# Kernel optimization log

Measured on AMD Instinct MI355X. Metric: run time of the kernel, lower is better.

Reference implementation:

```python
import jax, jax.numpy as jnp
import numpy as np

FP8_MAX = 448.0  # float8_e4m3 max finite value


def setup_inputs() -> dict:
    key = jax.random.key(0)
    k1, k2, k3, k4, k5 = jax.random.split(key, 5)
    B, S, IN, OUT = 8, 2048, 2048, 2048
    x = jax.random.normal(k1, (B, S, IN), dtype=jnp.float32)
    weight = jax.random.normal(k2, (OUT, IN), dtype=jnp.float32) * 0.02
    bias = jax.random.normal(k3, (OUT,), dtype=jnp.float32)
    # per-tensor scales, kept positive and away from zero
    scale_in = jax.random.uniform(k4, (1,), dtype=jnp.float32) * 0.09 + 0.01
    scale_w = jax.random.uniform(k5, (1,), dtype=jnp.float32) * 0.09 + 0.01
    return {"x": x, "weight": weight, "bias": bias,
            "scale_in": scale_in, "scale_w": scale_w}


def _fp8_quantize(x, scale):
    # divide by scale, saturate to fp8 range, cast to fp8 e4m3
    q = jnp.clip(x / scale, -FP8_MAX, FP8_MAX)
    return q.astype(jnp.float8_e4m3fn)


def reference(x, weight, bias, scale_in, scale_w):
    # quantize input and weight to fp8 (per-tensor scales)
    xq = _fp8_quantize(x, scale_in)            # [B,S,IN] fp8
    wq = _fp8_quantize(weight, scale_w)        # [OUT,IN] fp8
    # scaled matmul: accumulate in fp32, dequant with scale_a*scale_b, emit fp16
    acc = jnp.einsum('bsk,nk->bsn', xq.astype(jnp.float32), wq.astype(jnp.float32))
    out = (acc * (scale_in[0] * scale_w[0])).astype(jnp.float16)
    out = out + bias.astype(jnp.float16)       # trailing bias add at fp16
    return out
```

## Files before the change

### kernel.cpp

```cpp
#include <hip/hip_runtime.h>
#include <hip/hip_fp16.h>
#include <stdint.h>

#define MDIM 16384
#define NDIM 2048
#define KDIM 2048

typedef __attribute__((ext_vector_type(4))) float f32x4;
typedef __attribute__((ext_vector_type(4))) int   i32x4;
typedef __attribute__((ext_vector_type(8))) int   i32x8;

__device__ __forceinline__ unsigned f32_to_e4m3(float x) {
    float q = fminf(448.f, fmaxf(-448.f, x));
    unsigned ub = __float_as_uint(q);
    unsigned sgn = (ub >> 24) & 0x80u;
    float aq = fabsf(q);
    int E = (int)((__float_as_uint(aq) >> 23) & 0xff) - 127;
    if (E < -6) E = -6;
    float rq = __uint_as_float((unsigned)(130 - E) << 23);
    int m = (int)rintf(aq * rq);
    if (m == 16) { m = 8; E += 1; }
    unsigned bits;
    if (m < 8) bits = sgn | (unsigned)m;
    else       bits = sgn | ((unsigned)(E + 7) << 3) | (unsigned)(m - 8);
    return bits;
}

__device__ __forceinline__ void quant_span(const float* __restrict__ x,
                                           uint8_t* __restrict__ q, float sc,
                                           unsigned i0, unsigned stride,
                                           unsigned n16) {
    for (unsigned i = i0; i < n16; i += stride) {
        const float4* xp = (const float4*)(x + (size_t)i * 16);
        uint32_t w[4];
#pragma unroll
        for (int j = 0; j < 4; ++j) {
            float4 v = xp[j];
            unsigned b0 = f32_to_e4m3(v.x / sc);
            unsigned b1 = f32_to_e4m3(v.y / sc);
            unsigned b2 = f32_to_e4m3(v.z / sc);
            unsigned b3 = f32_to_e4m3(v.w / sc);
            w[j] = b0 | (b1 << 8) | (b2 << 16) | (b3 << 24);
        }
        ((uint4*)q)[i] = make_uint4(w[0], w[1], w[2], w[3]);
    }
}

__global__ void quant_both_kernel(const float* __restrict__ x,
                                  uint8_t* __restrict__ xq,
                                  const float* __restrict__ w,
                                  uint8_t* __restrict__ wq,
                                  const float* __restrict__ s_in,
                                  const float* __restrict__ s_w) {
    if (blockIdx.x < 2048) {
        unsigned i0 = blockIdx.x * blockDim.x + threadIdx.x;
        quant_span(x, xq, s_in[0], i0, 2048 * 256,
                   (unsigned)((size_t)MDIM * KDIM / 16));
    } else {
        unsigned i0 = (blockIdx.x - 2048) * blockDim.x + threadIdx.x;
        quant_span(w, wq, s_w[0], i0, 256 * 256,
                   (unsigned)((size_t)NDIM * KDIM / 16));
    }
}

#define BM 256
#define BN 256
#define BKB 128
#define NKT (KDIM / BKB)

__device__ __forceinline__ void gload_lds16(const uint8_t* g, uint8_t* l) {
    __builtin_amdgcn_global_load_lds(
        (const __attribute__((address_space(1))) void*)g,
        (__attribute__((address_space(3))) void*)l, 16, 0, 0);
}

__device__ __forceinline__ void barrier_fenced() {
    asm volatile("" ::: "memory");
    __builtin_amdgcn_s_barrier();
    asm volatile("" ::: "memory");
}

__global__ __launch_bounds__(512) void gemm_fp8_kernel(
    const uint8_t* __restrict__ Aq, const uint8_t* __restrict__ Bq,
    const float* __restrict__ bias, const float* __restrict__ s_in,
    const float* __restrict__ s_w, float* __restrict__ out) {

    extern __shared__ uint8_t lds[];

    int nwg = gridDim.x;
    int cpx = nwg >> 3;
    int bid = blockIdx.x;
    int swz = (bid & 7) * cpx + (bid >> 3);
    int tm = swz >> 3;
    int tn = swz & 7;
    int row0 = tm * BM;
    int col0 = tn * BN;

    int tid  = threadIdx.x;
    int lane = tid & 63;
    int wid  = tid >> 6;
    int wr = wid >> 2, wc = wid & 3;
    int r15 = lane & 15;
    int g   = lane >> 4;

    int perm0 = ((2 * g + r15) & 7) << 4;
    int perm1 = ((2 * g + 1 + r15) & 7) << 4;

    int pj[2] = {tid, 512 + tid};
    int rj[2], cj[2];
#pragma unroll
    for (int j = 0; j < 2; ++j) {
        rj[j] = pj[j] >> 3;
        cj[j] = ((pj[j] & 7) - (rj[j] & 7)) & 7;
    }
    size_t asrcoff[2], bsrcoff[2];
    int    adst[2], bdst[2];
#pragma unroll
    for (int j = 0; j < 2; ++j) {
        int ar = (rj[j] & 63) + ((rj[j] >> 6) << 7);
        asrcoff[j] = (size_t)ar * KDIM + cj[j] * 16;
        bsrcoff[j] = (size_t)rj[j] * KDIM + cj[j] * 16;
        adst[j] = pj[j] * 16;
        bdst[j] = 32768 + pj[j] * 16;
    }

    const uint8_t* Asrc = Aq + (size_t)row0 * KDIM;
    const uint8_t* Bsrc = Bq + (size_t)col0 * KDIM;

#define STAGE_A(U, KT, DST)                                                   \
    {                                                                         \
        _Pragma("unroll")                                                     \
        for (int j_ = 0; j_ < 2; ++j_)                                        \
            gload_lds16(Asrc + asrcoff[j_] + (size_t)(U) * 64 * KDIM +        \
                            (size_t)(KT) * BKB,                               \
                        (DST) + adst[j_] + (U) * 16384);                      \
    }
#define STAGE_B(U, KT, DST)                                                   \
    {                                                                         \
        _Pragma("unroll")                                                     \
        for (int j_ = 0; j_ < 2; ++j_)                                        \
            gload_lds16(Bsrc + bsrcoff[j_] + (size_t)(U) * 128 * KDIM +       \
                            (size_t)(KT) * BKB,                               \
                        (DST) + bdst[j_] + (U) * 16384);                      \
    }

    f32x4 acc[8][4];
#pragma unroll
    for (int m = 0; m < 8; ++m)
#pragma unroll
        for (int n = 0; n < 4; ++n)
            acc[m][n] = (f32x4){0.f, 0.f, 0.f, 0.f};

    {
        uint8_t* b0 = &lds[0];
        uint8_t* b1 = &lds[65536];
        STAGE_A(0, 0, b0); STAGE_B(0, 0, b0); STAGE_B(1, 0, b0); STAGE_A(1, 0, b0);
        STAGE_A(0, 1, b1); STAGE_B(0, 1, b1);
        asm volatile("s_waitcnt vmcnt(4)" ::: "memory");
        barrier_fenced();
    }

    int aRowBase = wr * 64;
    int bUnit = (wc >> 1) * 1024;
    int bRowBase = (wc & 1) * 64;

    i32x8 bf[4], af[4];

#define LOAD_BF(bo)                                                           \
    _Pragma("unroll")                                                         \
    for (int n_ = 0; n_ < 4; ++n_) {                                          \
        int rB = bRowBase + n_ * 16 + r15;                                    \
        const uint8_t* rp = lds + (bo) + 32768 + (bUnit + rB * 8) * 16;       \
        i32x4 lo = *(const i32x4*)(rp + perm0);                               \
        i32x4 hi = *(const i32x4*)(rp + perm1);                               \
        _Pragma("unroll")                                                     \
        for (int q_ = 0; q_ < 4; ++q_) { bf[n_][q_] = lo[q_]; bf[n_][4 + q_] = hi[q_]; } \
    }

#define LOAD_AF(bo, MH)                                                       \
    _Pragma("unroll")                                                         \
    for (int m_ = 0; m_ < 4; ++m_) {                                          \
        int rA = aRowBase + m_ * 16 + r15;                                    \
        const uint8_t* rp = lds + (bo) + ((MH) * 1024 + rA * 8) * 16;         \
        i32x4 lo = *(const i32x4*)(rp + perm0);                               \
        i32x4 hi = *(const i32x4*)(rp + perm1);                               \
        _Pragma("unroll")                                                     \
        for (int q_ = 0; q_ < 4; ++q_) { af[m_][q_] = lo[q_]; af[m_][4 + q_] = hi[q_]; } \
    }

#define MFMA_BLOCK(MH)                                                        \
    __builtin_amdgcn_s_setprio(1);                                            \
    _Pragma("unroll")                                                         \
    for (int m_ = 0; m_ < 4; ++m_)                                            \
        _Pragma("unroll")                                                     \
        for (int n_ = 0; n_ < 4; ++n_)                                        \
            acc[(MH) * 4 + m_][n_] =                                          \
                __builtin_amdgcn_mfma_scale_f32_16x16x128_f8f6f4(             \
                    af[m_], bf[n_], acc[(MH) * 4 + m_][n_],                   \
                    0, 0, 0, 127, 0, 127);                                    \
    __builtin_amdgcn_s_setprio(0);

    for (int t = 0; t < NKT; ++t) {
        const unsigned bo = (unsigned)(t & 1) << 16;
        uint8_t* nbuf = &lds[(unsigned)((t + 1) & 1) << 16];
        uint8_t* cbuf = &lds[bo];
        if (t + 1 < NKT) { STAGE_B(1, t + 1, nbuf); STAGE_A(1, t + 1, nbuf); }
        LOAD_BF(bo);
        LOAD_AF(bo, 0);
        MFMA_BLOCK(0);
        barrier_fenced();
        if (t + 2 < NKT) { STAGE_A(0, t + 2, cbuf); STAGE_B(0, t + 2, cbuf); }
        LOAD_AF(bo, 1);
        MFMA_BLOCK(1);
        if (t + 2 < NKT)      asm volatile("s_waitcnt vmcnt(4)" ::: "memory");
        else if (t + 1 < NKT) asm volatile("s_waitcnt vmcnt(0)" ::: "memory");
        barrier_fenced();
    }

    float s = s_in[0] * s_w[0];
    int g4 = g * 4;
#pragma unroll
    for (int n = 0; n < 4; ++n) {
        int col = col0 + wc * 64 + n * 16 + r15;
        __half hb = __float2half(bias[col]);
#pragma unroll
        for (int mh = 0; mh < 2; ++mh)
#pragma unroll
            for (int m = 0; m < 4; ++m) {
                int rbase = row0 + wr * 128 + mh * 64 + m * 16 + g4;
#pragma unroll
                for (int r = 0; r < 4; ++r) {
                    __half h = __float2half(acc[mh * 4 + m][n][r] * s);
                    out[(size_t)(rbase + r) * NDIM + col] =
                        __half2float(__hadd(h, hb));
                }
            }
    }
#undef STAGE_A
#undef STAGE_B
#undef LOAD_BF
#undef LOAD_AF
#undef MFMA_BLOCK
}

extern "C" void kernel_launch(void* const* d_in, const int* in_sizes, int n_in,
                              void* d_out, int out_size, void* d_ws, size_t ws_size,
                              hipStream_t stream) {
    const float* x      = (const float*)d_in[0];
    const float* weight = (const float*)d_in[1];
    const float* bias   = (const float*)d_in[2];
    const float* s_in   = (const float*)d_in[3];
    const float* s_w    = (const float*)d_in[4];
    float* out          = (float*)d_out;

    uint8_t* xq = (uint8_t*)d_ws;
    uint8_t* wq = (uint8_t*)d_ws + (size_t)MDIM * KDIM;

    quant_both_kernel<<<2304, 256, 0, stream>>>(x, xq, weight, wq, s_in, s_w);

    dim3 grid((MDIM / BM) * (NDIM / BN));
    gemm_fp8_kernel<<<grid, 512, 131072, stream>>>(xq, wq, bias, s_in, s_w, out);
}
```

Before: 119.6 us.

## Re-pipeline K loop with one-tile prefetch and stage epilogue through LDS

The main loop is restructured so the next K tile is prefetched into the other LDS buffer in pieces that are interleaved between quarter-sized MFMA groups, instead of a two-tiles-ahead split across buffer halves. B fragments are loaded in halves, and the waitcnt and barrier points are moved to match. The epilogue now writes scaled, bias-added results into an LDS slab and then stores full rows with 16-byte vector writes, replacing the strided per-element global stores. This adds extra barriers and LDS traffic in the epilogue, and the shorter prefetch distance may expose more global-load latency.

```diff
diff --git a/kernel.cpp b/kernel.cpp
--- a/kernel.cpp
+++ b/kernel.cpp
@@ -153,10 +153,8 @@
 
     {
         uint8_t* b0 = &lds[0];
-        uint8_t* b1 = &lds[65536];
-        STAGE_A(0, 0, b0); STAGE_B(0, 0, b0); STAGE_B(1, 0, b0); STAGE_A(1, 0, b0);
-        STAGE_A(0, 1, b1); STAGE_B(0, 1, b1);
-        asm volatile("s_waitcnt vmcnt(4)" ::: "memory");
+        STAGE_A(0, 0, b0); STAGE_B(1, 0, b0); STAGE_B(0, 0, b0); STAGE_A(1, 0, b0);
+        asm volatile("s_waitcnt vmcnt(2)" ::: "memory");
         barrier_fenced();
     }
 
@@ -166,9 +164,9 @@
 
     i32x8 bf[4], af[4];
 
-#define LOAD_BF(bo)                                                           \
+#define LOAD_BF_H(bo, H)                                                      \
     _Pragma("unroll")                                                         \
-    for (int n_ = 0; n_ < 4; ++n_) {                                          \
+    for (int n_ = 2 * (H); n_ < 2 * (H) + 2; ++n_) {                          \
         int rB = bRowBase + n_ * 16 + r15;                                    \
         const uint8_t* rp = lds + (bo) + 32768 + (bUnit + rB * 8) * 16;       \
         i32x4 lo = *(const i32x4*)(rp + perm0);                               \
@@ -188,12 +186,12 @@
         for (int q_ = 0; q_ < 4; ++q_) { af[m_][q_] = lo[q_]; af[m_][4 + q_] = hi[q_]; } \
     }
 
-#define MFMA_BLOCK(MH)                                                        \
+#define MFMA_Q(MH, NH)                                                        \
     __builtin_amdgcn_s_setprio(1);                                            \
     _Pragma("unroll")                                                         \
     for (int m_ = 0; m_ < 4; ++m_)                                            \
         _Pragma("unroll")                                                     \
-        for (int n_ = 0; n_ < 4; ++n_)                                        \
+        for (int n_ = 2 * (NH); n_ < 2 * (NH) + 2; ++n_)                      \
             acc[(MH) * 4 + m_][n_] =                                          \
                 __builtin_amdgcn_mfma_scale_f32_16x16x128_f8f6f4(             \
                     af[m_], bf[n_], acc[(MH) * 4 + m_][n_],                   \
@@ -202,45 +200,62 @@
 
     for (int t = 0; t < NKT; ++t) {
         const unsigned bo = (unsigned)(t & 1) << 16;
-        uint8_t* nbuf = &lds[(unsigned)((t + 1) & 1) << 16];
-        uint8_t* cbuf = &lds[bo];
-        if (t + 1 < NKT) { STAGE_B(1, t + 1, nbuf); STAGE_A(1, t + 1, nbuf); }
-        LOAD_BF(bo);
+        uint8_t* obuf = &lds[(unsigned)((t + 1) & 1) << 16];
         LOAD_AF(bo, 0);
-        MFMA_BLOCK(0);
-        barrier_fenced();
-        if (t + 2 < NKT) { STAGE_A(0, t + 2, cbuf); STAGE_B(0, t + 2, cbuf); }
+        LOAD_BF_H(bo, 0);
+        if (t + 1 < NKT) { STAGE_A(0, t + 1, obuf); STAGE_B(1, t + 1, obuf); }
+        MFMA_Q(0, 0);
+        LOAD_BF_H(bo, 1);
+        if (t + 1 < NKT) { STAGE_B(0, t + 1, obuf); }
+        MFMA_Q(0, 1);
+        if (t + 1 < NKT) asm volatile("s_waitcnt vmcnt(6)" ::: "memory");
+        else             asm volatile("s_waitcnt vmcnt(0)" ::: "memory");
+        barrier_fenced();
         LOAD_AF(bo, 1);
-        MFMA_BLOCK(1);
-        if (t + 2 < NKT)      asm volatile("s_waitcnt vmcnt(4)" ::: "memory");
-        else if (t + 1 < NKT) asm volatile("s_waitcnt vmcnt(0)" ::: "memory");
+        MFMA_Q(1, 0);
+        if (t + 1 < NKT) { STAGE_A(1, t + 1, obuf); }
+        MFMA_Q(1, 1);
+        if (t + 1 < NKT) asm volatile("s_waitcnt vmcnt(2)" ::: "memory");
         barrier_fenced();
     }
 
     float s = s_in[0] * s_w[0];
-    int g4 = g * 4;
-#pragma unroll
-    for (int n = 0; n < 4; ++n) {
-        int col = col0 + wc * 64 + n * 16 + r15;
-        __half hb = __float2half(bias[col]);
-#pragma unroll
-        for (int mh = 0; mh < 2; ++mh)
+    float* slab = (float*)lds;
+    __half hb[4];
+#pragma unroll
+    for (int n = 0; n < 4; ++n)
+        hb[n] = __float2half(bias[col0 + wc * 64 + n * 16 + r15]);
+
+#pragma unroll
+    for (int mh = 0; mh < 2; ++mh) {
+#pragma unroll
+        for (int n = 0; n < 4; ++n) {
+            int colb = wc * 64 + n * 16 + r15;
 #pragma unroll
             for (int m = 0; m < 4; ++m) {
-                int rbase = row0 + wr * 128 + mh * 64 + m * 16 + g4;
+                int sr = wr * 64 + m * 16 + g * 4;
 #pragma unroll
                 for (int r = 0; r < 4; ++r) {
                     __half h = __float2half(acc[mh * 4 + m][n][r] * s);
-                    out[(size_t)(rbase + r) * NDIM + col] =
-                        __half2float(__hadd(h, hb));
+                    slab[(sr + r) * 256 + colb] = __half2float(__hadd(h, hb[n]));
                 }
             }
+        }
+        barrier_fenced();
+#pragma unroll
+        for (int it = 0; it < 16; ++it) {
+            int srow = wid * 16 + it;
+            f32x4 vv = *(const f32x4*)&slab[srow * 256 + lane * 4];
+            int grow = row0 + (srow >> 6) * 128 + mh * 64 + (srow & 63);
+            *(f32x4*)&out[(size_t)grow * NDIM + col0 + lane * 4] = vv;
+        }
+        barrier_fenced();
     }
 #undef STAGE_A
 #undef STAGE_B
-#undef LOAD_BF
+#undef LOAD_BF_H
 #undef LOAD_AF
-#undef MFMA_BLOCK
+#undef MFMA_Q
 }
 
 extern "C" void kernel_launch(void* const* d_in, const int* in_sizes, int n_in,
```

Result: no change. 119.8 us (+0.1%).
